# Optimization experiments

Hardware: AMD Instinct MI355X
Metric: run time of the kernel (lower is better)

The kernel has to match this reference:

```python
import jax, jax.numpy as jnp
import numpy as np


def setup_inputs() -> dict:
    key = jax.random.key(0)
    kx, kwl, kbl, kwr = jax.random.split(key, 4)
    B = 64          # batch of identical DAGs
    L = 11          # number of levels (leaves = level 0)
    NPL = 10000     # nodes per level
    K = 16          # children per non-leaf node
    N = L * NPL     # 110000 nodes per graph
    # Build a layered DAG: edges go child (level l-1) -> father (level l),
    # matching the module's convention edge_index[0]=child, edge_index[1]=father
    # (leaves are nodes with in-degree 0).
    rng = np.random.default_rng(0)
    srcs, dsts = [], []
    for l in range(1, L):
        fathers = np.arange(l * NPL, (l + 1) * NPL)
        children = rng.integers((l - 1) * NPL, l * NPL, size=(NPL, K))
        srcs.append(children.reshape(-1))
        dsts.append(np.repeat(fathers, K))
    edge_index = jnp.asarray(
        np.stack([np.concatenate(srcs), np.concatenate(dsts)]), dtype=jnp.int32
    )  # [2, E] with E = (L-1)*NPL*K = 1.6M
    x = jax.random.normal(kx, (B, N, 1), dtype=jnp.float32)
    w_l = jax.random.normal(kwl, (1, 1), dtype=jnp.float32)   # lin_l weight (1->1)
    b_l = jax.random.normal(kbl, (1,), dtype=jnp.float32) * 0.1  # lin_l bias
    w_r = jax.random.normal(kwr, (1, 1), dtype=jnp.float32)   # lin_r weight (no bias)
    return {"x": x, "w_l": w_l, "b_l": b_l, "w_r": w_r,
            "edge_index": edge_index, "num_levels": L - 1}


def _dagprop(x, w_l, b_l, w_r, edge_index, num_levels):
    # x: [B, N, 1] scalar node features for B identical DAGs.
    src, dst = edge_index[0], edge_index[1]
    N = x.shape[1]
    xb = x[..., 0]  # [B, N]
    indeg = jnp.zeros((N,), jnp.int32).at[dst].add(1)  # in-degree (children count)
    is_leaf = indeg == 0
    # Init: out[leaves] = tanh(x[leaves]); out[non-leaves] = lin_r(x) (no bias).
    out = jnp.where(is_leaf[None, :], jnp.tanh(xb), xb * w_r[0, 0])  # [B, N]
    visited = is_leaf
    inv_deg = 1.0 / jnp.maximum(indeg, 1).astype(xb.dtype)
    for _ in range(num_levels):
        # fathers whose children are ALL visited become the next frontier
        nvis = jnp.zeros((N,), jnp.int32).at[dst].add(visited[src].astype(jnp.int32))
        ready = (~visited) & (indeg > 0) & (nvis == indeg)
        # scatter-mean of children's outputs over all incoming edges (aggr='mean');
        # only consumed at 'ready' nodes, whose children are all visited.
        agg = jnp.zeros_like(out).at[:, dst].add(out[:, src]) * inv_deg[None, :]
        # out[next] = tanh(out[next] + lin_l(agg[next]))
        new = jnp.tanh(out + agg * w_l[0, 0] + b_l[0])
        out = jnp.where(ready[None, :], new, out)
        visited = visited | ready
    return out[..., None]  # [B, N, 1]


def reference(x, w_l, b_l, w_r, edge_index, num_levels):
    return _dagprop(x, w_l, b_l, w_r, edge_index, num_levels)
```

## Files before the change

kernel.cpp:

```cpp
#include <hip/hip_runtime.h>
#include <math.h>

#define BATCH  64
#define NPL    10000
#define NLEV   10
#define NNODE  110000
#define KCH    16
#define GSPLIT 8
#define FPB    (NPL / GSPLIT)
#define THREADS 512
#define ITER    3

#define EXPITCH_F4 3072
#define EXPITCH_F  (EXPITCH_F4 * 4)
#define EXCH_FLOATS (2 * BATCH * EXPITCH_F)
#define CNT_STRIDE 16

__device__ inline void coh_store(float* p, float v) {
    __hip_atomic_store(p, v, __ATOMIC_RELAXED, __HIP_MEMORY_SCOPE_AGENT);
}

__device__ inline void coh_load4_x6(const float4* p0, const float4* p1,
                                    const float4* p2, const float4* p3,
                                    const float4* p4, const float4* p5,
                                    float4& a, float4& b, float4& c,
                                    float4& d, float4& e, float4& f) {
    asm volatile("global_load_dwordx4 %0, %6, off sc0 sc1\n\t"
                 "global_load_dwordx4 %1, %7, off sc0 sc1\n\t"
                 "global_load_dwordx4 %2, %8, off sc0 sc1\n\t"
                 "global_load_dwordx4 %3, %9, off sc0 sc1\n\t"
                 "global_load_dwordx4 %4, %10, off sc0 sc1\n\t"
                 "global_load_dwordx4 %5, %11, off sc0 sc1\n\t"
                 "s_waitcnt vmcnt(0)"
                 : "=&v"(a), "=&v"(b), "=&v"(c), "=&v"(d), "=&v"(e), "=&v"(f)
                 : "v"(p0), "v"(p1), "v"(p2), "v"(p3), "v"(p4), "v"(p5)
                 : "memory");
}

__global__ __launch_bounds__(THREADS, 4) void k_dag_split(
    const float* __restrict__ x,
    float*       __restrict__ out,
    const int4*  __restrict__ src4,
    float*       __restrict__ exch,
    int*         __restrict__ cnt,
    const float* __restrict__ wl_p,
    const float* __restrict__ bl_p,
    const float* __restrict__ wr_p)
{
    __shared__ float buf[EXPITCH_F];
    const int b   = blockIdx.x >> 3;
    const int q   = blockIdx.x & 7;
    const int tid = threadIdx.x;
    const float wr   = wr_p[0];
    const float wl16 = wl_p[0] * (1.0f / 16.0f);
    const float bl   = bl_p[0];
    const float* __restrict__ xb = x   + (size_t)b * NNODE;
    float*       __restrict__ ob = out + (size_t)b * NNODE;
    const int f0 = q * FPB;
    int* mycnt = cnt + b * CNT_STRIDE;

    int4 pf[ITER][4];

    {
        float* ex0 = exch + (size_t)b * EXPITCH_F;
        for (int i = f0 + tid; i < f0 + FPB; i += THREADS) {
            float v = tanhf(xb[i]);
            ob[i] = v;
            coh_store(ex0 + i, v);
        }
    }
    {
        __syncthreads();
#pragma unroll
        for (int it = 0; it < ITER; ++it) {
            int f = tid + it * THREADS;
            int fe = (f < FPB) ? f : (FPB - 1);
            const int4* p = src4 + (size_t)(f0 + fe) * (KCH / 4);
#pragma unroll
            for (int j = 0; j < 4; ++j) pf[it][j] = p[j];
        }
        if (tid == 0) {
            __hip_atomic_fetch_add(mycnt, 1, __ATOMIC_RELAXED, __HIP_MEMORY_SCOPE_AGENT);
            while (__hip_atomic_load(mycnt, __ATOMIC_RELAXED, __HIP_MEMORY_SCOPE_AGENT) < GSPLIT)
                __builtin_amdgcn_s_sleep(1);
        }
        asm volatile("" ::: "memory");
        __syncthreads();
    }

    for (int l = 1; l <= NLEV; ++l) {
        {
            const float4* exr4 = (const float4*)(exch +
                ((size_t)((l - 1) & 1) * BATCH + b) * EXPITCH_F);
            float4 va, vb, vc, vd, ve, vf;
            coh_load4_x6(exr4 + tid,        exr4 + tid + 512,
                         exr4 + tid + 1024, exr4 + tid + 1536,
                         exr4 + tid + 2048, exr4 + tid + 2560,
                         va, vb, vc, vd, ve, vf);
            float4* bufv = (float4*)buf;
            bufv[tid]        = va;  bufv[tid + 512]  = vb;
            bufv[tid + 1024] = vc;  bufv[tid + 1536] = vd;
            bufv[tid + 2048] = ve;  bufv[tid + 2560] = vf;
        }
        __syncthreads();

        const int off   = (l - 1) * NPL;
        const int nodeb = l * NPL + f0;
        float* exw = exch + ((size_t)(l & 1) * BATCH + b) * EXPITCH_F + f0;
#pragma unroll
        for (int it = 0; it < ITER; ++it) {
            const int f = tid + it * THREADS;
            if (f < FPB) {
                const int4 c0 = pf[it][0];
                const int4 c1 = pf[it][1];
                const int4 c2 = pf[it][2];
                const int4 c3 = pf[it][3];
                float s = buf[c0.x - off] + buf[c0.y - off]
                        + buf[c0.z - off] + buf[c0.w - off]
                        + buf[c1.x - off] + buf[c1.y - off]
                        + buf[c1.z - off] + buf[c1.w - off]
                        + buf[c2.x - off] + buf[c2.y - off]
                        + buf[c2.z - off] + buf[c2.w - off]
                        + buf[c3.x - off] + buf[c3.y - off]
                        + buf[c3.z - off] + buf[c3.w - off];
                const float v = tanhf(fmaf(s, wl16, fmaf(xb[nodeb + f], wr, bl)));
                ob[nodeb + f] = v;
                if (l < NLEV) coh_store(exw + f, v);
            }
        }
        if (l < NLEV) {
            __syncthreads();
            const int4* nsrc = src4 + (size_t)(l * NPL + f0) * (KCH / 4);
#pragma unroll
            for (int it = 0; it < ITER; ++it) {
                int f = tid + it * THREADS;
                int fe = (f < FPB) ? f : (FPB - 1);
                const int4* p = nsrc + (size_t)fe * (KCH / 4);
#pragma unroll
                for (int j = 0; j < 4; ++j) pf[it][j] = p[j];
            }
            if (tid == 0) {
                __hip_atomic_fetch_add(mycnt, 1, __ATOMIC_RELAXED, __HIP_MEMORY_SCOPE_AGENT);
                while (__hip_atomic_load(mycnt, __ATOMIC_RELAXED, __HIP_MEMORY_SCOPE_AGENT) < GSPLIT * (l + 1))
                    __builtin_amdgcn_s_sleep(1);
            }
            asm volatile("" ::: "memory");
            __syncthreads();
        }
    }
}

extern "C" void kernel_launch(void* const* d_in, const int* in_sizes, int n_in,
                              void* d_out, int out_size, void* d_ws, size_t ws_size,
                              hipStream_t stream) {
    const float* x  = (const float*)d_in[0];
    const float* wl = (const float*)d_in[1];
    const float* bl = (const float*)d_in[2];
    const float* wr = (const float*)d_in[3];
    const int*   ei = (const int*)d_in[4];

    const int4* src4 = (const int4*)ei;
    float* out  = (float*)d_out;
    float* exch = (float*)d_ws;
    int*   cnt  = (int*)((char*)d_ws + EXCH_FLOATS * sizeof(float));

    hipMemsetAsync(cnt, 0, BATCH * CNT_STRIDE * sizeof(int), stream);
    k_dag_split<<<BATCH * GSPLIT, THREADS, 0, stream>>>(
        x, out, src4, exch, cnt, wl, bl, wr);
}
```

Baseline: 163.4 us.

## Process graph pairs per block with byte-flag barriers and shared index loads

Each block now handles two batch graphs at once, using 1024 threads and two shared-memory buffers. The child index lists are loaded once and reused for both graphs, which halves index traffic. The counter-based barrier is replaced by per-level byte flags polled as one 64-bit word, and the index prefetch that overlapped the barrier is dropped. Risks: the grid halves to 256 blocks of 1024 threads with double the shared memory, which lowers occupancy and parallelism, and index loads now sit on the critical path after each barrier.

Result: faster. 153.6 us (-6.0%).

```diff
diff --git a/kernel.cpp b/kernel.cpp
--- a/kernel.cpp
+++ b/kernel.cpp
@@ -8,16 +8,24 @@
 #define KCH    16
 #define GSPLIT 8
 #define FPB    (NPL / GSPLIT)
-#define THREADS 512
-#define ITER    3
+#define NPAIR  (BATCH / 2)
+#define THREADS 1024
+#define ITER    2
 
 #define EXPITCH_F4 3072
 #define EXPITCH_F  (EXPITCH_F4 * 4)
 #define EXCH_FLOATS (2 * BATCH * EXPITCH_F)
-#define CNT_STRIDE 16
+#define FLAG_STRIDE 128
 
 __device__ inline void coh_store(float* p, float v) {
     __hip_atomic_store(p, v, __ATOMIC_RELAXED, __HIP_MEMORY_SCOPE_AGENT);
+}
+__device__ inline void flag_set(unsigned char* p) {
+    __hip_atomic_store(p, (unsigned char)1, __ATOMIC_RELAXED,
+                       __HIP_MEMORY_SCOPE_AGENT);
+}
+__device__ inline unsigned long long flag_poll(const unsigned long long* p) {
+    return __hip_atomic_load(p, __ATOMIC_RELAXED, __HIP_MEMORY_SCOPE_AGENT);
 }
 
 __device__ inline void coh_load4_x6(const float4* p0, const float4* p1,
@@ -37,115 +45,115 @@
                  : "memory");
 }
 
-__global__ __launch_bounds__(THREADS, 4) void k_dag_split(
+__global__ __launch_bounds__(THREADS, 4) void k_dag_pair(
     const float* __restrict__ x,
     float*       __restrict__ out,
     const int4*  __restrict__ src4,
     float*       __restrict__ exch,
-    int*         __restrict__ cnt,
+    unsigned char* __restrict__ flags,
     const float* __restrict__ wl_p,
     const float* __restrict__ bl_p,
     const float* __restrict__ wr_p)
 {
-    __shared__ float buf[EXPITCH_F];
-    const int b   = blockIdx.x >> 3;
-    const int q   = blockIdx.x & 7;
-    const int tid = threadIdx.x;
+    __shared__ float bufA[EXPITCH_F];
+    __shared__ float bufB[EXPITCH_F];
+    const int blk  = blockIdx.x;
+    const int pair = blk >> 3;
+    const int q    = blk & 7;
+    const int gA   = pair * 2, gB = gA + 1;
+    const int tid  = threadIdx.x;
     const float wr   = wr_p[0];
     const float wl16 = wl_p[0] * (1.0f / 16.0f);
     const float bl   = bl_p[0];
-    const float* __restrict__ xb = x   + (size_t)b * NNODE;
-    float*       __restrict__ ob = out + (size_t)b * NNODE;
+    const float* __restrict__ xA = x   + (size_t)gA * NNODE;
+    const float* __restrict__ xB = x   + (size_t)gB * NNODE;
+    float*       __restrict__ oA = out + (size_t)gA * NNODE;
+    float*       __restrict__ oB = out + (size_t)gB * NNODE;
     const int f0 = q * FPB;
-    int* mycnt = cnt + b * CNT_STRIDE;
-
-    int4 pf[ITER][4];
+    unsigned long long* flA = (unsigned long long*)(flags + gA * FLAG_STRIDE);
+    unsigned long long* flB = (unsigned long long*)(flags + gB * FLAG_STRIDE);
+    const unsigned long long ALL = 0x0101010101010101ULL;
 
     {
-        float* ex0 = exch + (size_t)b * EXPITCH_F;
+        float* exA0 = exch + (size_t)gA * EXPITCH_F;
+        float* exB0 = exch + (size_t)gB * EXPITCH_F;
         for (int i = f0 + tid; i < f0 + FPB; i += THREADS) {
-            float v = tanhf(xb[i]);
-            ob[i] = v;
-            coh_store(ex0 + i, v);
+            float vA = tanhf(xA[i]); oA[i] = vA; coh_store(exA0 + i, vA);
+            float vB = tanhf(xB[i]); oB[i] = vB; coh_store(exB0 + i, vB);
         }
     }
-    {
-        __syncthreads();
-#pragma unroll
-        for (int it = 0; it < ITER; ++it) {
-            int f = tid + it * THREADS;
-            int fe = (f < FPB) ? f : (FPB - 1);
-            const int4* p = src4 + (size_t)(f0 + fe) * (KCH / 4);
-#pragma unroll
-            for (int j = 0; j < 4; ++j) pf[it][j] = p[j];
-        }
-        if (tid == 0) {
-            __hip_atomic_fetch_add(mycnt, 1, __ATOMIC_RELAXED, __HIP_MEMORY_SCOPE_AGENT);
-            while (__hip_atomic_load(mycnt, __ATOMIC_RELAXED, __HIP_MEMORY_SCOPE_AGENT) < GSPLIT)
-                __builtin_amdgcn_s_sleep(1);
-        }
-        asm volatile("" ::: "memory");
-        __syncthreads();
+    __syncthreads();
+    if (tid == 0) {
+        flag_set((unsigned char*)flA + 0 * 8 + q);
+        flag_set((unsigned char*)flB + 0 * 8 + q);
     }
 
     for (int l = 1; l <= NLEV; ++l) {
+        const int pprev = (l - 1) & 1;
+        if (tid == 0)
+            while (flag_poll(flA + (l - 1)) != ALL) __builtin_amdgcn_s_sleep(1);
+        if (tid == 256)
+            while (flag_poll(flB + (l - 1)) != ALL) __builtin_amdgcn_s_sleep(1);
+        asm volatile("" ::: "memory");
+        __syncthreads();
+
         {
-            const float4* exr4 = (const float4*)(exch +
-                ((size_t)((l - 1) & 1) * BATCH + b) * EXPITCH_F);
-            float4 va, vb, vc, vd, ve, vf;
-            coh_load4_x6(exr4 + tid,        exr4 + tid + 512,
-                         exr4 + tid + 1024, exr4 + tid + 1536,
-                         exr4 + tid + 2048, exr4 + tid + 2560,
-                         va, vb, vc, vd, ve, vf);
-            float4* bufv = (float4*)buf;
-            bufv[tid]        = va;  bufv[tid + 512]  = vb;
-            bufv[tid + 1024] = vc;  bufv[tid + 1536] = vd;
-            bufv[tid + 2048] = ve;  bufv[tid + 2560] = vf;
+            const float4* eA = (const float4*)(exch +
+                ((size_t)pprev * BATCH + gA) * EXPITCH_F);
+            const float4* eB = (const float4*)(exch +
+                ((size_t)pprev * BATCH + gB) * EXPITCH_F);
+            float4 a0, a1, a2, b0, b1, b2;
+            coh_load4_x6(eA + tid, eA + tid + 1024, eA + tid + 2048,
+                         eB + tid, eB + tid + 1024, eB + tid + 2048,
+                         a0, a1, a2, b0, b1, b2);
+            float4* vA = (float4*)bufA;  float4* vB = (float4*)bufB;
+            vA[tid] = a0; vA[tid + 1024] = a1; vA[tid + 2048] = a2;
+            vB[tid] = b0; vB[tid + 1024] = b1; vB[tid + 2048] = b2;
         }
         __syncthreads();
 
         const int off   = (l - 1) * NPL;
         const int nodeb = l * NPL + f0;
-        float* exw = exch + ((size_t)(l & 1) * BATCH + b) * EXPITCH_F + f0;
+        float* ewA = exch + ((size_t)(l & 1) * BATCH + gA) * EXPITCH_F + f0;
+        float* ewB = exch + ((size_t)(l & 1) * BATCH + gB) * EXPITCH_F + f0;
+        const int4* sp = src4 + (size_t)((l - 1) * NPL + f0) * (KCH / 4);
 #pragma unroll
         for (int it = 0; it < ITER; ++it) {
             const int f = tid + it * THREADS;
             if (f < FPB) {
-                const int4 c0 = pf[it][0];
-                const int4 c1 = pf[it][1];
-                const int4 c2 = pf[it][2];
-                const int4 c3 = pf[it][3];
-                float s = buf[c0.x - off] + buf[c0.y - off]
-                        + buf[c0.z - off] + buf[c0.w - off]
-                        + buf[c1.x - off] + buf[c1.y - off]
-                        + buf[c1.z - off] + buf[c1.w - off]
-                        + buf[c2.x - off] + buf[c2.y - off]
-                        + buf[c2.z - off] + buf[c2.w - off]
-                        + buf[c3.x - off] + buf[c3.y - off]
-                        + buf[c3.z - off] + buf[c3.w - off];
-                const float v = tanhf(fmaf(s, wl16, fmaf(xb[nodeb + f], wr, bl)));
-                ob[nodeb + f] = v;
-                if (l < NLEV) coh_store(exw + f, v);
+                const int4 c0 = sp[f * 4 + 0];
+                const int4 c1 = sp[f * 4 + 1];
+                const int4 c2 = sp[f * 4 + 2];
+                const int4 c3 = sp[f * 4 + 3];
+                float sA = bufA[c0.x - off] + bufA[c0.y - off]
+                         + bufA[c0.z - off] + bufA[c0.w - off]
+                         + bufA[c1.x - off] + bufA[c1.y - off]
+                         + bufA[c1.z - off] + bufA[c1.w - off]
+                         + bufA[c2.x - off] + bufA[c2.y - off]
+                         + bufA[c2.z - off] + bufA[c2.w - off]
+                         + bufA[c3.x - off] + bufA[c3.y - off]
+                         + bufA[c3.z - off] + bufA[c3.w - off];
+                float sB = bufB[c0.x - off] + bufB[c0.y - off]
+                         + bufB[c0.z - off] + bufB[c0.w - off]
+                         + bufB[c1.x - off] + bufB[c1.y - off]
+                         + bufB[c1.z - off] + bufB[c1.w - off]
+                         + bufB[c2.x - off] + bufB[c2.y - off]
+                         + bufB[c2.z - off] + bufB[c2.w - off]
+                         + bufB[c3.x - off] + bufB[c3.y - off]
+                         + bufB[c3.z - off] + bufB[c3.w - off];
+                const float vA = tanhf(fmaf(sA, wl16, fmaf(xA[nodeb + f], wr, bl)));
+                const float vB = tanhf(fmaf(sB, wl16, fmaf(xB[nodeb + f], wr, bl)));
+                oA[nodeb + f] = vA;
+                oB[nodeb + f] = vB;
+                if (l < NLEV) { coh_store(ewA + f, vA); coh_store(ewB + f, vB); }
             }
         }
         if (l < NLEV) {
             __syncthreads();
-            const int4* nsrc = src4 + (size_t)(l * NPL + f0) * (KCH / 4);
-#pragma unroll
-            for (int it = 0; it < ITER; ++it) {
-                int f = tid + it * THREADS;
-                int fe = (f < FPB) ? f : (FPB - 1);
-                const int4* p = nsrc + (size_t)fe * (KCH / 4);
-#pragma unroll
-                for (int j = 0; j < 4; ++j) pf[it][j] = p[j];
+            if (tid == 0) {
+                flag_set((unsigned char*)flA + l * 8 + q);
+                flag_set((unsigned char*)flB + l * 8 + q);
             }
-            if (tid == 0) {
-                __hip_atomic_fetch_add(mycnt, 1, __ATOMIC_RELAXED, __HIP_MEMORY_SCOPE_AGENT);
-                while (__hip_atomic_load(mycnt, __ATOMIC_RELAXED, __HIP_MEMORY_SCOPE_AGENT) < GSPLIT * (l + 1))
-                    __builtin_amdgcn_s_sleep(1);
-            }
-            asm volatile("" ::: "memory");
-            __syncthreads();
         }
     }
 }
@@ -162,9 +170,9 @@
     const int4* src4 = (const int4*)ei;
     float* out  = (float*)d_out;
     float* exch = (float*)d_ws;
-    int*   cnt  = (int*)((char*)d_ws + EXCH_FLOATS * sizeof(float));
+    unsigned char* flags = (unsigned char*)d_ws + (size_t)EXCH_FLOATS * sizeof(float);
 
-    hipMemsetAsync(cnt, 0, BATCH * CNT_STRIDE * sizeof(int), stream);
-    k_dag_split<<<BATCH * GSPLIT, THREADS, 0, stream>>>(
-        x, out, src4, exch, cnt, wl, bl, wr);
+    hipMemsetAsync(flags, 0, BATCH * FLAG_STRIDE, stream);
+    k_dag_pair<<<NPAIR * GSPLIT, THREADS, 0, stream>>>(
+        x, out, src4, exch, flags, wl, bl, wr);
 }
```
